# Performance work log

Measured on AMD Instinct MI355X. Metric: run time of the kernel, lower is better.

## Reference

```python
import jax, jax.numpy as jnp
import numpy as np

N_H, N_O, D = 5000, 15000, 1024
E_HH, E_OO, E_HO = 20000, 40000, 40000


def setup_inputs() -> dict:
    key = jax.random.key(0)
    ks = jax.random.split(key, 20)
    N = N_H + N_O
    w = lambda k, shp: jax.random.normal(k, shp, dtype=jnp.float32) * 0.02
    inp = {
        'n_f': jax.random.normal(ks[0], (N, D), dtype=jnp.float32),
        'src_hh': jax.random.randint(ks[1], (E_HH,), 0, N_H),
        'dst_hh': jax.random.randint(ks[2], (E_HH,), 0, N_H),
        'src_oo': jax.random.randint(ks[3], (E_OO,), 0, N_O) + N_H,
        'dst_oo': jax.random.randint(ks[4], (E_OO,), 0, N_O) + N_H,
        'src_ho': jax.random.randint(ks[5], (E_HO,), 0, N_H),
        'dst_ho': jax.random.randint(ks[6], (E_HO,), 0, N_O) + N_H,
        'W_hh': w(ks[7], (2 * D, D)), 'b_hh': jnp.zeros((D,), jnp.float32),
        'W_oo': w(ks[8], (2 * D, D)), 'b_oo': jnp.zeros((D,), jnp.float32),
        'W_ho': w(ks[9], (2 * D, D)), 'b_ho': jnp.zeros((D,), jnp.float32),
        'W_att': w(ks[10], (D, 1)), 'b_att': jnp.zeros((1,), jnp.float32),
        'W_hn': w(ks[11], (2 * D, D)), 'b_hn': jnp.zeros((D,), jnp.float32),
        'W_on': w(ks[12], (2 * D, D)), 'b_on': jnp.zeros((D,), jnp.float32),
    }
    return inp


def reference(n_f, src_hh, dst_hh, src_oo, dst_oo, src_ho, dst_ho,
              W_hh, b_hh, W_oo, b_oo, W_ho, b_ho, W_att, b_att,
              W_hn, b_hn, W_on, b_on):
    N = n_f.shape[0]

    def edge_mlp(src, dst, W, b):
        # gather -> concat -> Linear -> ReLU  (H_H/O_O/H_O EdgeApplyModule)
        feat = jnp.concatenate([n_f[src], n_f[dst]], axis=1)  # [E, 2D]
        return jax.nn.relu(feat @ W + b)                       # [E, D]

    e_f = jnp.concatenate([
        edge_mlp(src_hh, dst_hh, W_hh, b_hh),
        edge_mlp(src_oo, dst_oo, W_oo, b_oo),
        edge_mlp(src_ho, dst_ho, W_ho, b_ho),
    ], axis=0)                                                 # [E, D]
    src = jnp.concatenate([src_hh, src_oo, src_ho])
    dst = jnp.concatenate([dst_hh, dst_oo, dst_ho])

    # E_AttentionModule: per-edge scalar attention logit
    a = (e_f @ W_att + b_att)[:, 0]                            # [E]

    # update_all: per-destination softmax over incoming edges (mailbox softmax)
    seg_max = jax.ops.segment_max(a, dst, num_segments=N)
    seg_max = jnp.where(jnp.isfinite(seg_max), seg_max, 0.0)
    ex = jnp.exp(a - seg_max[dst])
    denom = jax.ops.segment_sum(ex, dst, num_segments=N)
    alpha = ex / jnp.where(denom[dst] == 0, 1.0, denom[dst])   # [E]
    z = jax.ops.segment_sum(alpha[:, None] * n_f[src], dst, num_segments=N)  # [N, D]

    # Node apply: concat(n_f, z_f) -> Linear -> ReLU, separate h/o MLPs
    new_h = jax.nn.relu(jnp.concatenate([n_f[:N_H], z[:N_H]], axis=1) @ W_hn + b_hn)
    new_o = jax.nn.relu(jnp.concatenate([n_f[N_H:], z[N_H:]], axis=1) @ W_on + b_on)
    return jnp.concatenate([new_h, new_o], axis=0)             # [N, D] new_n_f
```

## Files before the change

### kernel.cpp

```cpp
#include <hip/hip_runtime.h>

#define N_H   5000
#define N_O   15000
#define N_TOT 20000
#define DD    1024
#define E_HH  20000
#define E_OO  40000
#define E_HO  40000
#define E_TOT 100000

typedef unsigned short u16;
typedef unsigned int u32;
typedef __attribute__((ext_vector_type(8))) short short8;
typedef __attribute__((ext_vector_type(4))) float f32x4;
typedef const __attribute__((address_space(1))) u32 gas_u32;
typedef __attribute__((address_space(3))) u32 las_u32;

__device__ __forceinline__ float bf2f(u16 u) {
    union { unsigned int i; float f; } v; v.i = ((unsigned int)u) << 16; return v.f;
}
__device__ __forceinline__ u16 f2bf(float f) {
    union { float f; unsigned int i; } v; v.f = f;
    unsigned int u = v.i;
    return (u16)((u + 0x7FFFu + ((u >> 16) & 1u)) >> 16);
}

#define CAST_NB 10000
#define CAT_NB  391
#define TW_NB   10240
struct TW  { const float* W; u16* dT; u16* dB; int ld; };
struct TW5 { TW t[5]; };
__global__ void cast_cat_tw(const float* __restrict__ in, u16* __restrict__ out,
                            const int* __restrict__ shh, const int* __restrict__ dhh,
                            const int* __restrict__ soo, const int* __restrict__ doo,
                            const int* __restrict__ sho, const int* __restrict__ dho,
                            int* __restrict__ src_all, int* __restrict__ dst_all,
                            int* __restrict__ deg, TW5 p) {
    __shared__ float tile[32][33];
    int b = blockIdx.x;
    if (b < CAST_NB) {
        size_t i = ((size_t)b * 256 + threadIdx.x) * 8;
        float4 a = *(const float4*)(in + i);
        float4 c = *(const float4*)(in + i + 4);
        u16 o[8] = {f2bf(a.x), f2bf(a.y), f2bf(a.z), f2bf(a.w),
                    f2bf(c.x), f2bf(c.y), f2bf(c.z), f2bf(c.w)};
        *(uint4*)(out + i) = *(const uint4*)o;
        return;
    }
    if (b < CAST_NB + CAT_NB) {
        int e = (b - CAST_NB) * 256 + threadIdx.x;
        if (e >= E_TOT) return;
        int s, d;
        if (e < E_HH)              { s = shh[e];               d = dhh[e]; }
        else if (e < E_HH + E_OO)  { s = soo[e - E_HH];        d = doo[e - E_HH]; }
        else                       { s = sho[e - E_HH - E_OO]; d = dho[e - E_HH - E_OO]; }
        src_all[e] = s; dst_all[e] = d;
        atomicAdd(&deg[d], 1);
        return;
    }
    int tb = b - CAST_NB - CAT_NB;
    int z = tb >> 10;
    int rem = tb & 1023;
    int bk = rem & 31, bn = rem >> 5;
    TW tw = p.t[z >> 1];
    int half = z & 1;
    int tx = threadIdx.x & 31, ty = threadIdx.x >> 5;
#pragma unroll
    for (int yy = 0; yy < 4; yy++) {
        int k = half * 1024 + bk * 32 + ty + yy * 8;
        int n = bn * 32 + tx;
        tile[ty + yy * 8][tx] = tw.W[(size_t)k * 1024 + n];
    }
    __syncthreads();
    u16* dst = half ? tw.dB : tw.dT;
#pragma unroll
    for (int yy = 0; yy < 4; yy++) {
        int n = bn * 32 + ty + yy * 8;
        int k = bk * 32 + tx;
        dst[(size_t)n * tw.ld + k] = f2bf(tile[tx][ty + yy * 8]);
    }
}

#define PROJ_NBM_H 40
#define PROJ_NBM_O 118
#define PROJ_NBN   24
__launch_bounds__(256)
__global__ void gemm_proj(const u16* __restrict__ Ah, const u16* __restrict__ Ao,
                          const u16* __restrict__ Bth, const u16* __restrict__ Bto,
                          u16* __restrict__ Ch, u16* __restrict__ Co) {
    __shared__ u16 smem[2][128][64];
    int bid = blockIdx.x;
    const u16* A; const u16* Bt; u16* C; int M;
    if (bid < PROJ_NBM_H * PROJ_NBN) { A = Ah; Bt = Bth; C = Ch; M = N_H; }
    else { bid -= PROJ_NBM_H * PROJ_NBN; A = Ao; Bt = Bto; C = Co; M = N_O; }
    int bm = bid / PROJ_NBN, bn = bid % PROJ_NBN;
    int t = threadIdx.x;
    int wave = t >> 6, lane = t & 63;
    int wr = wave >> 1, wc = wave & 1;
    int lm = lane & 15, q = lane >> 4;
    f32x4 acc[4][4] = {};
    int srow = lane >> 3;
    int scol = ((lane & 7) ^ srow) * 8;

    for (int k0 = 0; k0 < 1024; k0 += 64) {
#pragma unroll
        for (int it = 0; it < 4; it++) {
            int chunk = wave * 4 + it;
            int row = chunk * 8 + srow;
            int gr = bm * 128 + row; if (gr >= M) gr = M - 1;
            __builtin_amdgcn_global_load_lds((gas_u32*)(A + (size_t)gr * 1024 + k0 + scol),
                                             (las_u32*)&smem[0][chunk * 8][0], 16, 0, 0);
            __builtin_amdgcn_global_load_lds((gas_u32*)(Bt + (size_t)(bn * 128 + row) * 1024 + k0 + scol),
                                             (las_u32*)&smem[1][chunk * 8][0], 16, 0, 0);
        }
        __syncthreads();
#pragma unroll
        for (int ks = 0; ks < 64; ks += 32) {
            short8 af[4], bfr[4];
            int pc = (((ks >> 3) + q) ^ (lm & 7)) * 8;
#pragma unroll
            for (int i = 0; i < 4; i++)
                af[i] = *(const short8*)&smem[0][wr * 64 + i * 16 + lm][pc];
#pragma unroll
            for (int j = 0; j < 4; j++)
                bfr[j] = *(const short8*)&smem[1][wc * 64 + j * 16 + lm][pc];
#pragma unroll
            for (int i = 0; i < 4; i++)
#pragma unroll
                for (int j = 0; j < 4; j++)
                    acc[i][j] = __builtin_amdgcn_mfma_f32_16x16x32_bf16(af[i], bfr[j], acc[i][j], 0, 0, 0);
        }
        __syncthreads();
    }
    u16* sc = &smem[0][0][0];
#pragma unroll
    for (int i = 0; i < 4; i++)
#pragma unroll
        for (int j = 0; j < 4; j++)
#pragma unroll
            for (int r = 0; r < 4; r++)
                sc[(wr * 64 + i * 16 + q * 4 + r) * 128 + (wc * 64 + j * 16 + lm)] =
                    f2bf(acc[i][j][r]);
    __syncthreads();
#pragma unroll
    for (int it = 0; it < 8; it++) {
        int flat = it * 256 + t;
        int r = flat >> 4, cs = (flat & 15) * 8;
        int grow = bm * 128 + r;
        if (grow < M)
            *(uint4*)&C[(size_t)grow * 3072 + bn * 128 + cs] = *(const uint4*)&sc[r * 128 + cs];
    }
}

#define NODE_NBM_H 40
#define NODE_NBM_O 118
#define NODE_NBN   8
__launch_bounds__(256)
__global__ void gemm_node(const u16* __restrict__ nf_h, const u16* __restrict__ nf_o,
                          const u16* __restrict__ z_h, const u16* __restrict__ z_o,
                          const u16* __restrict__ Bthn, const u16* __restrict__ Bton,
                          const float* __restrict__ b_hn, const float* __restrict__ b_on,
                          float* __restrict__ out_h, float* __restrict__ out_o) {
    __shared__ u16 smem[2][128][64];
    int bid = (blockIdx.x & 7) * ((NODE_NBM_H + NODE_NBM_O) * NODE_NBN / 8)
            + (blockIdx.x >> 3);
    const u16 *A0, *A1, *Bt; const float* bias; float* C; int M;
    if (bid < NODE_NBM_H * NODE_NBN) {
        A0 = nf_h; A1 = z_h; Bt = Bthn; bias = b_hn; C = out_h; M = N_H;
    } else {
        bid -= NODE_NBM_H * NODE_NBN;
        A0 = nf_o; A1 = z_o; Bt = Bton; bias = b_on; C = out_o; M = N_O;
    }
    int bm = bid / NODE_NBN, bn = bid % NODE_NBN;
    int t = threadIdx.x;
    int wave = t >> 6, lane = t & 63;
    int wr = wave >> 1, wc = wave & 1;
    int lm = lane & 15, q = lane >> 4;
    f32x4 acc[4][4] = {};
    int srow = lane >> 3;
    int scol = ((lane & 7) ^ srow) * 8;

    for (int half = 0; half < 2; half++) {
        const u16* Asrc = half ? A1 : A0;
        const u16* Bth = Bt + half * 1024;
        for (int k0 = 0; k0 < 1024; k0 += 64) {
#pragma unroll
            for (int it = 0; it < 4; it++) {
                int chunk = wave * 4 + it;
                int row = chunk * 8 + srow;
                int gr = bm * 128 + row; if (gr >= M) gr = M - 1;
                __builtin_amdgcn_global_load_lds((gas_u32*)(Asrc + (size_t)gr * 1024 + k0 + scol),
                                                 (las_u32*)&smem[0][chunk * 8][0], 16, 0, 0);
                __builtin_amdgcn_global_load_lds((gas_u32*)(Bth + (size_t)(bn * 128 + row) * 2048 + k0 + scol),
                                                 (las_u32*)&smem[1][chunk * 8][0], 16, 0, 0);
            }
            __syncthreads();
#pragma unroll
            for (int ks = 0; ks < 64; ks += 32) {
                short8 af[4], bfr[4];
                int pc = (((ks >> 3) + q) ^ (lm & 7)) * 8;
#pragma unroll
                for (int i = 0; i < 4; i++)
                    af[i] = *(const short8*)&smem[0][wr * 64 + i * 16 + lm][pc];
#pragma unroll
                for (int j = 0; j < 4; j++)
                    bfr[j] = *(const short8*)&smem[1][wc * 64 + j * 16 + lm][pc];
#pragma unroll
                for (int i = 0; i < 4; i++)
#pragma unroll
                    for (int j = 0; j < 4; j++)
                        acc[i][j] = __builtin_amdgcn_mfma_f32_16x16x32_bf16(af[i], bfr[j], acc[i][j], 0, 0, 0);
            }
            __syncthreads();
        }
    }
    float* sf = (float*)&smem[0][0][0];
#pragma unroll
    for (int p = 0; p < 2; p++) {
        if (p) __syncthreads();
        if (wr == p) {
#pragma unroll
            for (int j = 0; j < 4; j++) {
                int col = wc * 64 + j * 16 + lm;
                float bv = bias[bn * 128 + col];
#pragma unroll
                for (int i = 0; i < 4; i++)
#pragma unroll
                    for (int r = 0; r < 4; r++)
                        sf[(i * 16 + q * 4 + r) * 128 + col] =
                            fmaxf(acc[i][j][r] + bv, 0.0f);
            }
        }
        __syncthreads();
#pragma unroll
        for (int it = 0; it < 8; it++) {
            int c = it * 256 + t;
            int rl = c >> 5, k4 = c & 31;
            int grow = bm * 128 + p * 64 + rl;
            if (grow < M)
                *(float4*)&C[(size_t)grow * 1024 + bn * 128 + k4 * 4] =
                    *(const float4*)&sf[rl * 128 + k4 * 4];
        }
    }
}

__global__ void edge_att(const u16* __restrict__ proj_h, const u16* __restrict__ proj_o,
                         const float* __restrict__ b_hh, const float* __restrict__ b_oo,
                         const float* __restrict__ b_ho,
                         const float* __restrict__ W_att, const float* __restrict__ b_att,
                         const int* __restrict__ src_all, const int* __restrict__ dst_all,
                         float* __restrict__ a_out) {
    int wave = threadIdx.x >> 6, lane = threadIdx.x & 63;
    int e0 = blockIdx.x * 64 + wave * 16;
    if (e0 >= E_TOT) return;
    const float* bsel = (e0 < E_HH) ? b_hh : (e0 < E_HH + E_OO ? b_oo : b_ho);
    float ww[16], bb[16];
#pragma unroll
    for (int i = 0; i < 16; i++) { ww[i] = W_att[lane * 16 + i]; bb[i] = bsel[lane * 16 + i]; }
    float batt = b_att[0];
    for (int k = 0; k < 16; k++) {
        int e = e0 + k;
        int s = src_all[e], d = dst_all[e];
        const u16 *u, *v;
        if (e < E_HH) {
            u = proj_h + (size_t)s * 3072;
            v = proj_h + (size_t)d * 3072 + 1024;
        } else if (e < E_HH + E_OO) {
            u = proj_o + (size_t)(s - N_H) * 3072;
            v = proj_o + (size_t)(d - N_H) * 3072 + 1024;
        } else {
            u = proj_h + (size_t)s * 3072 + 2048;
            v = proj_o + (size_t)(d - N_H) * 3072 + 2048;
        }
        int off = lane * 16;
        uint4 u0 = *(const uint4*)(u + off), u1 = *(const uint4*)(u + off + 8);
        uint4 v0 = *(const uint4*)(v + off), v1 = *(const uint4*)(v + off + 8);
        const u16* pu0 = (const u16*)&u0; const u16* pu1 = (const u16*)&u1;
        const u16* pv0 = (const u16*)&v0; const u16* pv1 = (const u16*)&v1;
        float acc = 0.f;
#pragma unroll
        for (int i = 0; i < 8; i++) {
            float tv = bf2f(pu0[i]) + bf2f(pv0[i]) + bb[i];
            acc += fmaxf(tv, 0.f) * ww[i];
        }
#pragma unroll
        for (int i = 0; i < 8; i++) {
            float tv = bf2f(pu1[i]) + bf2f(pv1[i]) + bb[8 + i];
            acc += fmaxf(tv, 0.f) * ww[8 + i];
        }
#pragma unroll
        for (int o = 32; o > 0; o >>= 1) acc += __shfl_down(acc, o);
        if (lane == 0) a_out[e] = acc + batt;
    }
}

__global__ void scan_deg(const int* __restrict__ deg, int* __restrict__ indptr) {
    __shared__ int sums[1024];
    int t = threadIdx.x;
    const int CH = 20;
    int beg = t * CH, end = beg + CH;
    if (end > N_TOT) end = N_TOT;
    if (beg > N_TOT) beg = N_TOT;
    int s = 0;
    for (int i = beg; i < end; i++) s += deg[i];
    sums[t] = s;
    __syncthreads();
    for (int off = 1; off < 1024; off <<= 1) {
        int v = sums[t];
        int add = (t >= off) ? sums[t - off] : 0;
        __syncthreads();
        sums[t] = v + add;
        __syncthreads();
    }
    int run = (t == 0) ? 0 : sums[t - 1];
    for (int i = beg; i < end; i++) { indptr[i] = run; run += deg[i]; }
    if (t == 1023) indptr[N_TOT] = sums[1023];
}

__global__ void fill_csr(const int* __restrict__ dst_all, const int* __restrict__ indptr,
                         int* __restrict__ cursor, int* __restrict__ edge_ids) {
    int e = blockIdx.x * 256 + threadIdx.x;
    if (e < E_TOT) {
        int d = dst_all[e];
        int pos = atomicAdd(&cursor[d], 1);
        edge_ids[indptr[d] + pos] = e;
    }
}

#define MAXDEG 1024
__global__ void soft_z(const float* __restrict__ a, const int* __restrict__ indptr,
                       const int* __restrict__ edge_ids, const int* __restrict__ src_all,
                       const u16* __restrict__ nf, u16* __restrict__ z) {
    __shared__ float s_a[MAXDEG];
    __shared__ int   s_src[MAXDEG];
    __shared__ float s_inv;
    int node = blockIdx.x;
    int t = threadIdx.x;
    int beg = indptr[node], end = indptr[node + 1];
    int deg = end - beg; if (deg > MAXDEG) deg = MAXDEG;
    if (t < 64) {
        float m = -1e30f;
        for (int i = t; i < deg; i += 64) {
            int eid = edge_ids[beg + i];
            float av = a[eid];
            s_a[i] = av;
            s_src[i] = src_all[eid];
            if (av > m) m = av;
        }
        for (int o = 32; o > 0; o >>= 1) m = fmaxf(m, __shfl_down(m, o));
        m = __shfl(m, 0);
        float ssum = 0.f;
        for (int i = t; i < deg; i += 64) {
            float ex = __expf(s_a[i] - m);
            s_a[i] = ex;
            ssum += ex;
        }
        for (int o = 32; o > 0; o >>= 1) ssum += __shfl_down(ssum, o);
        if (t == 0) s_inv = (ssum > 0.f) ? 1.0f / ssum : 0.f;
    }
    __syncthreads();
    float a0 = 0.f, a1 = 0.f, a2 = 0.f, a3 = 0.f;
    int base = t * 4;
    float inv = s_inv;
    for (int i = 0; i < deg; i++) {
        float al = s_a[i] * inv;
        const u16* row = nf + (size_t)s_src[i] * DD + base;
        uint2 p = *(const uint2*)row;
        const u16* pp = (const u16*)&p;
        a0 += al * bf2f(pp[0]); a1 += al * bf2f(pp[1]);
        a2 += al * bf2f(pp[2]); a3 += al * bf2f(pp[3]);
    }
    uint2 ov;
    u16* po = (u16*)&ov;
    po[0] = f2bf(a0); po[1] = f2bf(a1); po[2] = f2bf(a2); po[3] = f2bf(a3);
    *(uint2*)(z + (size_t)node * DD + base) = ov;
}

extern "C" void kernel_launch(void* const* d_in, const int* in_sizes, int n_in,
                              void* d_out, int out_size, void* d_ws, size_t ws_size,
                              hipStream_t stream) {
    const float* nf   = (const float*)d_in[0];
    const int* shh    = (const int*)d_in[1];
    const int* dhh    = (const int*)d_in[2];
    const int* soo    = (const int*)d_in[3];
    const int* doo    = (const int*)d_in[4];
    const int* sho    = (const int*)d_in[5];
    const int* dho    = (const int*)d_in[6];
    const float* W_hh = (const float*)d_in[7];
    const float* b_hh = (const float*)d_in[8];
    const float* W_oo = (const float*)d_in[9];
    const float* b_oo = (const float*)d_in[10];
    const float* W_ho = (const float*)d_in[11];
    const float* b_ho = (const float*)d_in[12];
    const float* W_att= (const float*)d_in[13];
    const float* b_att= (const float*)d_in[14];
    const float* W_hn = (const float*)d_in[15];
    const float* b_hn = (const float*)d_in[16];
    const float* W_on = (const float*)d_in[17];
    const float* b_on = (const float*)d_in[18];
    float* out = (float*)d_out;

    char* ws = (char*)d_ws;
    size_t off = 0;
    auto alloc = [&](size_t bytes) -> char* {
        char* p = ws + off;
        off += (bytes + 255) & ~(size_t)255;
        return p;
    };
    u16* nf_bf = (u16*)alloc((size_t)N_TOT * DD * 2);
    u16* Bt_h  = (u16*)alloc((size_t)3072 * 1024 * 2);
    u16* Bt_o  = (u16*)alloc((size_t)3072 * 1024 * 2);
    u16* Bt_hn = (u16*)alloc((size_t)1024 * 2048 * 2);
    u16* Bt_on = (u16*)alloc((size_t)1024 * 2048 * 2);
    u16* proj_h = (u16*)alloc((size_t)N_H * 3072 * 2);
    u16* proj_o = (u16*)alloc((size_t)N_O * 3072 * 2);
    u16* z_bf   = proj_h;
    float* a_log  = (float*)alloc(E_TOT * 4);
    int* src_all  = (int*)alloc(E_TOT * 4);
    int* dst_all  = (int*)alloc(E_TOT * 4);
    int* deg      = (int*)alloc(2 * N_TOT * 4);
    int* cursor   = deg + N_TOT;
    int* indptr   = (int*)alloc((N_TOT + 1) * 4);
    int* edge_ids = (int*)alloc(E_TOT * 4);
    (void)ws_size; (void)in_sizes; (void)n_in; (void)out_size;

    hipMemsetAsync(deg, 0, 2 * N_TOT * 4, stream);
    TW5 tws;
    tws.t[0] = {W_hh, Bt_h,                       Bt_h + (size_t)1024 * 1024, 1024};
    tws.t[1] = {W_oo, Bt_o,                       Bt_o + (size_t)1024 * 1024, 1024};
    tws.t[2] = {W_ho, Bt_h + (size_t)2048 * 1024, Bt_o + (size_t)2048 * 1024, 1024};
    tws.t[3] = {W_hn, Bt_hn,                      Bt_hn + 1024,               2048};
    tws.t[4] = {W_on, Bt_on,                      Bt_on + 1024,               2048};
    cast_cat_tw<<<CAST_NB + CAT_NB + TW_NB, 256, 0, stream>>>(
        nf, nf_bf, shh, dhh, soo, doo, sho, dho, src_all, dst_all, deg, tws);

    const u16* nf_bf_o = nf_bf + (size_t)N_H * DD;
    gemm_proj<<<(PROJ_NBM_H + PROJ_NBM_O) * PROJ_NBN, 256, 0, stream>>>(
        nf_bf, nf_bf_o, Bt_h, Bt_o, proj_h, proj_o);

    edge_att<<<(E_TOT + 63) / 64, 256, 0, stream>>>(proj_h, proj_o, b_hh, b_oo, b_ho,
                                                    W_att, b_att, src_all, dst_all, a_log);

    scan_deg<<<1, 1024, 0, stream>>>(deg, indptr);
    fill_csr<<<(E_TOT + 255) / 256, 256, 0, stream>>>(dst_all, indptr, cursor, edge_ids);

    soft_z<<<N_TOT, 256, 0, stream>>>(a_log, indptr, edge_ids, src_all, nf_bf, z_bf);

    gemm_node<<<(NODE_NBM_H + NODE_NBM_O) * NODE_NBN, 256, 0, stream>>>(
        nf_bf, nf_bf_o, z_bf, z_bf + (size_t)N_H * DD, Bt_hn, Bt_on,
        b_hn, b_on, out, out + (size_t)N_H * DD);
}
```

Measured before the change: 591.7 us.

## Assign one wavefront per node in softmax-aggregate kernel with online softmax

Replaces the block-per-node softmax/aggregation kernel with a wave-per-node kernel, so each block handles four destination nodes. The max and sum are computed in a single pass with an online-softmax combine over wave shuffles, which removes the shared-memory staging and __syncthreads. Each lane accumulates 16 features using 128-bit loads instead of 4 features with 64-bit loads. The cost is that the exponentials are recomputed in the aggregation loop and edge ids and sources are reloaded serially. Fewer threads are in flight per node, and per-wave work becomes imbalanced with node degree.

New measurement: 579.1 us. 1.02x faster.

```diff
diff --git a/kernel.cpp b/kernel.cpp
--- a/kernel.cpp
+++ b/kernel.cpp
@@ -327,53 +327,51 @@
     }
 }
 
-#define MAXDEG 1024
-__global__ void soft_z(const float* __restrict__ a, const int* __restrict__ indptr,
-                       const int* __restrict__ edge_ids, const int* __restrict__ src_all,
-                       const u16* __restrict__ nf, u16* __restrict__ z) {
-    __shared__ float s_a[MAXDEG];
-    __shared__ int   s_src[MAXDEG];
-    __shared__ float s_inv;
-    int node = blockIdx.x;
-    int t = threadIdx.x;
-    int beg = indptr[node], end = indptr[node + 1];
-    int deg = end - beg; if (deg > MAXDEG) deg = MAXDEG;
-    if (t < 64) {
-        float m = -1e30f;
-        for (int i = t; i < deg; i += 64) {
-            int eid = edge_ids[beg + i];
-            float av = a[eid];
-            s_a[i] = av;
-            s_src[i] = src_all[eid];
-            if (av > m) m = av;
-        }
-        for (int o = 32; o > 0; o >>= 1) m = fmaxf(m, __shfl_down(m, o));
-        m = __shfl(m, 0);
-        float ssum = 0.f;
-        for (int i = t; i < deg; i += 64) {
-            float ex = __expf(s_a[i] - m);
-            s_a[i] = ex;
-            ssum += ex;
-        }
-        for (int o = 32; o > 0; o >>= 1) ssum += __shfl_down(ssum, o);
-        if (t == 0) s_inv = (ssum > 0.f) ? 1.0f / ssum : 0.f;
-    }
-    __syncthreads();
-    float a0 = 0.f, a1 = 0.f, a2 = 0.f, a3 = 0.f;
-    int base = t * 4;
-    float inv = s_inv;
+__launch_bounds__(256)
+__global__ void soft_z_w(const float* __restrict__ a, const int* __restrict__ indptr,
+                         const int* __restrict__ edge_ids, const int* __restrict__ src_all,
+                         const u16* __restrict__ nf, u16* __restrict__ z) {
+    int wave = threadIdx.x >> 6, lane = threadIdx.x & 63;
+    int node = blockIdx.x * 4 + wave;
+    if (node >= N_TOT) return;
+    int beg = indptr[node];
+    int deg = indptr[node + 1] - beg;
+    float m = -1e30f, ssum = 0.f;
+    for (int i = lane; i < deg; i += 64) {
+        float av = a[edge_ids[beg + i]];
+        if (av > m) { ssum *= __expf(m - av); m = av; }
+        ssum += __expf(av - m);
+    }
+#pragma unroll
+    for (int o = 32; o > 0; o >>= 1) {
+        float m2 = __shfl_xor(m, o);
+        float s2 = __shfl_xor(ssum, o);
+        float mn = fmaxf(m, m2);
+        ssum = ssum * __expf(m - mn) + s2 * __expf(m2 - mn);
+        m = mn;
+    }
+    float inv = (ssum > 0.f) ? 1.0f / ssum : 0.f;
+    float av16[16] = {};
+    int base = lane * 16;
     for (int i = 0; i < deg; i++) {
-        float al = s_a[i] * inv;
-        const u16* row = nf + (size_t)s_src[i] * DD + base;
-        uint2 p = *(const uint2*)row;
-        const u16* pp = (const u16*)&p;
-        a0 += al * bf2f(pp[0]); a1 += al * bf2f(pp[1]);
-        a2 += al * bf2f(pp[2]); a3 += al * bf2f(pp[3]);
-    }
-    uint2 ov;
-    u16* po = (u16*)&ov;
-    po[0] = f2bf(a0); po[1] = f2bf(a1); po[2] = f2bf(a2); po[3] = f2bf(a3);
-    *(uint2*)(z + (size_t)node * DD + base) = ov;
+        int eid = edge_ids[beg + i];
+        float al = __expf(a[eid] - m) * inv;
+        const u16* row = nf + (size_t)src_all[eid] * DD + base;
+        uint4 p0 = *(const uint4*)row;
+        uint4 p1 = *(const uint4*)(row + 8);
+        const u16* pp0 = (const u16*)&p0;
+        const u16* pp1 = (const u16*)&p1;
+#pragma unroll
+        for (int j = 0; j < 8; j++) av16[j]     += al * bf2f(pp0[j]);
+#pragma unroll
+        for (int j = 0; j < 8; j++) av16[8 + j] += al * bf2f(pp1[j]);
+    }
+    u16 ov[16];
+#pragma unroll
+    for (int j = 0; j < 16; j++) ov[j] = f2bf(av16[j]);
+    const uint4* po = (const uint4*)ov;
+    *(uint4*)(z + (size_t)node * DD + base)     = po[0];
+    *(uint4*)(z + (size_t)node * DD + base + 8) = po[1];
 }
 
 extern "C" void kernel_launch(void* const* d_in, const int* in_sizes, int n_in,
@@ -444,7 +442,7 @@
     scan_deg<<<1, 1024, 0, stream>>>(deg, indptr);
     fill_csr<<<(E_TOT + 255) / 256, 256, 0, stream>>>(dst_all, indptr, cursor, edge_ids);
 
-    soft_z<<<N_TOT, 256, 0, stream>>>(a_log, indptr, edge_ids, src_all, nf_bf, z_bf);
+    soft_z_w<<<N_TOT / 4, 256, 0, stream>>>(a_log, indptr, edge_ids, src_all, nf_bf, z_bf);
 
     gemm_node<<<(NODE_NBM_H + NODE_NBM_O) * NODE_NBN, 256, 0, stream>>>(
         nf_bf, nf_bf_o, z_bf, z_bf + (size_t)N_H * DD, Bt_hn, Bt_on,
```
